# Kernel tuning notes

Hardware: AMD Instinct MI355X
Metric: run time of the kernel (lower is better)

## Reference

```python
import jax, jax.numpy as jnp
import numpy as np

V, T, E, HID = 32000, 48, 128, 256
B, L = 256, 512
H = HID // 2  # per-direction LSTM hidden


def setup_inputs() -> dict:
    key = jax.random.key(0)
    ks = jax.random.split(key, 16)
    lengths = jax.random.randint(ks[0], (B,), L // 2, L + 1)
    mask = (jnp.arange(L)[None, :] < lengths[:, None])  # (B, L) bool, step 0 always on
    words = jax.random.randint(ks[1], (B, L), 1, V).astype(jnp.int32)
    words = jnp.where(mask, words, 0)  # padding_idx = 0
    tags = jax.random.randint(ks[2], (B, L), 0, T).astype(jnp.int32)
    s = 0.1
    emb = jax.random.normal(ks[3], (V, E), jnp.float32) * s
    emb = emb.at[0].set(0.0)  # padding_idx row zeroed
    Wih_f = jax.random.normal(ks[4], (4 * H, E), jnp.float32) * s
    Whh_f = jax.random.normal(ks[5], (4 * H, H), jnp.float32) * s
    bih_f = jax.random.normal(ks[6], (4 * H,), jnp.float32) * s
    bhh_f = jax.random.normal(ks[7], (4 * H,), jnp.float32) * s
    Wih_b = jax.random.normal(ks[8], (4 * H, E), jnp.float32) * s
    Whh_b = jax.random.normal(ks[9], (4 * H, H), jnp.float32) * s
    bih_b = jax.random.normal(ks[10], (4 * H,), jnp.float32) * s
    bhh_b = jax.random.normal(ks[11], (4 * H,), jnp.float32) * s
    Wout = jax.random.normal(ks[12], (T, HID), jnp.float32) * s
    bout = jax.random.normal(ks[13], (T,), jnp.float32) * s
    trans = jax.random.normal(ks[14], (T, T), jnp.float32) * s
    se = jax.random.normal(ks[15], (2, T), jnp.float32) * s
    return dict(words=words, tags=tags, mask=mask, emb=emb,
                Wih_f=Wih_f, Whh_f=Whh_f, bih_f=bih_f, bhh_f=bhh_f,
                Wih_b=Wih_b, Whh_b=Whh_b, bih_b=bih_b, bhh_b=bhh_b,
                Wout=Wout, bout=bout, trans=trans,
                start_trans=se[0], end_trans=se[1])


def _lstm_dir(x, Wih, Whh, bih, bhh, reverse):
    # x: (L, B, E) -> hs: (L, B, H); PyTorch gate order i, f, g, o
    Lx, Bx, _ = x.shape
    Hx = Whh.shape[1]
    def step(carry, xt):
        h, c = carry
        g = xt @ Wih.T + h @ Whh.T + (bih + bhh)
        i, f, gg, o = jnp.split(g, 4, axis=-1)
        c = jax.nn.sigmoid(f) * c + jax.nn.sigmoid(i) * jnp.tanh(gg)
        h = jax.nn.sigmoid(o) * jnp.tanh(c)
        return (h, c), h
    init = (jnp.zeros((Bx, Hx), x.dtype), jnp.zeros((Bx, Hx), x.dtype))
    _, hs = jax.lax.scan(step, init, x, reverse=reverse)
    return hs


def reference(words, tags, mask, emb, Wih_f, Whh_f, bih_f, bhh_f,
              Wih_b, Whh_b, bih_b, bhh_b, Wout, bout, trans,
              start_trans, end_trans):
    Bn = words.shape[0]
    # --- features: embedding -> BiLSTM -> linear ---
    x = emb[words].transpose(1, 0, 2)          # (L, B, E)
    h_f = _lstm_dir(x, Wih_f, Whh_f, bih_f, bhh_f, reverse=False)
    h_b = _lstm_dir(x, Wih_b, Whh_b, bih_b, bhh_b, reverse=True)
    h = jnp.concatenate([h_f, h_b], axis=-1)   # (L, B, 2H)
    emis = h @ Wout.T + bout                   # (L, B, T)
    mT = mask.T                                # (L, B) bool
    mF = mT.astype(emis.dtype)
    tT = tags.T.astype(jnp.int32)              # (L, B)

    # --- CRF numerator: score of gold path ---
    barange = jnp.arange(Bn)
    num0 = start_trans[tT[0]] + emis[0, barange, tT[0]]
    def num_step(score, inp):
        em_t, tag_prev, tag_t, m_t = inp
        step_score = trans[tag_prev, tag_t] + em_t[barange, tag_t]
        return score + step_score * m_t, None
    num, _ = jax.lax.scan(num_step, num0, (emis[1:], tT[:-1], tT[1:], mF[1:]))
    seq_ends = mF.sum(0).astype(jnp.int32) - 1
    last_tags = tT[seq_ends, barange]
    num = num + end_trans[last_tags]

    # --- CRF denominator: forward algorithm (logsumexp recurrence) ---
    den0 = start_trans[None, :] + emis[0]      # (B, T)
    def den_step(score, inp):
        em_t, m_t = inp
        nxt = jax.nn.logsumexp(score[:, :, None] + trans[None] + em_t[:, None, :], axis=1)
        return jnp.where(m_t[:, None], nxt, score), None
    den, _ = jax.lax.scan(den_step, den0, (emis[1:], mT[1:]))
    denom = jax.nn.logsumexp(den + end_trans[None, :], axis=1)

    llh = num - denom
    return -llh.mean()  # reduction='mean', negated
```

## Files before the change

kernel.cpp:

```cpp
#include <hip/hip_runtime.h>
#include <hip/hip_bf16.h>

typedef unsigned short ushort_t;
typedef unsigned int uint_t;
typedef __bf16 bf16x8 __attribute__((ext_vector_type(8)));
typedef float f32x4 __attribute__((ext_vector_type(4)));

#define L2E 1.44269504088896340736f
#define LN2 0.69314718055994530942f

#define WGBAR() __asm__ volatile("s_waitcnt lgkmcnt(0)\n\ts_barrier" ::: "memory")

static __device__ __forceinline__ float fexp2(float x) { return __builtin_amdgcn_exp2f(x); }
static __device__ __forceinline__ float flog2(float x) { return __builtin_amdgcn_logf(x); }
static __device__ __forceinline__ float frcp (float x) { return __builtin_amdgcn_rcpf(x); }

static __device__ __forceinline__ float sigm(float x) {
  return frcp(1.0f + fexp2(-L2E * x));
}
static __device__ __forceinline__ float tanha(float x) {
  return 1.0f - 2.0f * frcp(1.0f + fexp2(2.0f * L2E * x));
}

static __device__ __forceinline__ uint_t cvtpk(float lo, float hi) {
  uint_t r;
  asm("v_cvt_pk_bf16_f32 %0, %1, %2" : "=v"(r) : "v"(lo), "v"(hi));
  return r;
}
static __device__ __forceinline__ bf16x8 pack8(float4 a, float4 b) {
  uint4 u = make_uint4(cvtpk(a.x, a.y), cvtpk(a.z, a.w),
                       cvtpk(b.x, b.y), cvtpk(b.z, b.w));
  return __builtin_bit_cast(bf16x8, u);
}
static __device__ __forceinline__ uint2 pack4(float4 a) {
  return make_uint2(cvtpk(a.x, a.y), cvtpk(a.z, a.w));
}

template <int K>
static __device__ __forceinline__ float rotk(float x) {
  if constexpr (K == 0) {
    return x;
  } else {
    return __builtin_bit_cast(float, __builtin_amdgcn_update_dpp(
        0, __builtin_bit_cast(int, x), 0x120 + K, 0xf, 0xf, true));
  }
}

__global__ __launch_bounds__(512, 2) void k2_lstm(
    const int* __restrict__ words, const float* __restrict__ emb,
    const float* __restrict__ Wih_f, const float* __restrict__ Whh_f,
    const float* __restrict__ bih_f, const float* __restrict__ bhh_f,
    const float* __restrict__ Wih_b, const float* __restrict__ Whh_b,
    const float* __restrict__ bih_b, const float* __restrict__ bhh_b,
    ushort_t* __restrict__ hT, float* __restrict__ loss_out) {
  const int wg = blockIdx.x;
  const int dir = wg >> 7;
  const int r0 = (wg & 127) << 1;
  if (wg == 0 && threadIdx.x == 0) loss_out[0] = 0.f;
  const float* Whh = dir ? Whh_b : Whh_f;
  const float* Wih = dir ? Wih_b : Wih_f;
  const float* bih = dir ? bih_b : bih_f;
  const float* bhh = dir ? bhh_b : bhh_f;

  const int tid = threadIdx.x;
  const int w = tid >> 6;
  const int lane = tid & 63;
  const int l15 = lane & 15;
  const int kq = lane >> 4;

  __shared__ __align__(16) ushort_t hx[2][2][136];
  __shared__ __align__(16) ushort_t xp[2][16][128][4];
  __shared__ __align__(16) ushort_t xs[2][16][136];

  bf16x8 wfh[4][4], wfx[4][4];
  float biasP[4];
#pragma unroll
  for (int Q = 0; Q < 4; ++Q) {
    const int n = Q * 128 + w * 16 + l15;
    biasP[Q] = bih[n] + bhh[n];
#pragma unroll
    for (int c = 0; c < 4; ++c) {
      const int k0 = c * 32 + kq * 8;
      const float* sh = Whh + n * 128 + k0;
      const float* sx = Wih + n * 128 + k0;
      wfh[Q][c] = pack8(*(const float4*)sh, *(const float4*)(sh + 4));
      wfx[Q][c] = pack8(*(const float4*)sx, *(const float4*)(sx + 4));
    }
  }

  const int ur = (lane >> 4) & 1;
  const int uj = w * 16 + l15;
  float cst = 0.f;
  const f32x4 fz = {0.f, 0.f, 0.f, 0.f};

  const int sm = tid >> 5;
  const int sc = (tid & 31) * 4;
  const int str = r0 + (sm & 1);
  const int stl = sm >> 1;

  uint_t pd0[4], pd1[4];
  f32x4 pc = {0.f, 0.f, 0.f, 0.f};
  f32x4 pcsv = {0.f, 0.f, 0.f, 0.f};

  if (tid < 256) hx[0][tid >> 7][tid & 127] = 0;
  {
    const int tg = stl;
    const int tf = dir ? (511 - tg) : tg;
    const int word = words[str * 512 + tf];
    float4 av = *(const float4*)(emb + (size_t)word * 128 + sc);
    *(uint2*)&xs[1][sm][sc] = pack4(av);
  }
  WGBAR();
  {
    f32x4 qv[4];
#pragma unroll
    for (int Q = 0; Q < 4; ++Q) {
      f32x4 pc0 = {biasP[Q], biasP[Q], biasP[Q], biasP[Q]};
#pragma unroll
      for (int c = 0; c < 4; ++c) {
        bf16x8 af = __builtin_bit_cast(bf16x8, *(const uint4*)&xs[1][l15][kq * 8 + c * 32]);
        pc0 = __builtin_amdgcn_mfma_f32_16x16x32_bf16(af, wfx[Q][c], pc0, 0, 0, 0);
      }
      qv[Q] = pc0;
    }
#pragma unroll
    for (int rr = 0; rr < 4; ++rr) {
      pd0[rr] = cvtpk(qv[0][rr], qv[1][rr]);
      pd1[rr] = cvtpk(qv[2][rr], qv[3][rr]);
      *(uint2*)&xp[0][kq * 4 + rr][uj][0] = make_uint2(pd0[rr], pd1[rr]);
    }
  }
  {
    const int tg = 8 + stl;
    const int tf = dir ? (511 - tg) : tg;
    const int word = words[str * 512 + tf];
    float4 av = *(const float4*)(emb + (size_t)word * 128 + sc);
    *(uint2*)&xs[0][sm][sc] = pack4(av);
  }
  WGBAR();

  int sword = 0;
  float4 se0 = make_float4(0.f, 0.f, 0.f, 0.f);

#pragma unroll 1
  for (int i = 0; i < 64; ++i) {
    const int pcon = i & 1;
    const int ppro = pcon ^ 1;
    bf16x8 afp[4];
    if (i < 63) {
#pragma unroll
      for (int c = 0; c < 4; ++c)
        afp[c] = __builtin_bit_cast(bf16x8, *(const uint4*)&xs[pcon][l15][kq * 8 + c * 32]);
    }
#pragma unroll
    for (int s = 0; s < 8; ++s) {
      const int t = i * 8 + s;
      const int p = t & 1;
      const uint2 xq = *(const uint2*)&xp[pcon][2 * s + ur][uj][0];
      if (i < 62) {
        if (s == 0) {
          const int tg = (i + 2) * 8 + stl;
          const int tf = dir ? (511 - tg) : tg;
          sword = words[str * 512 + tf];
        }
        if (s == 2) se0 = *(const float4*)(emb + (size_t)sword * 128 + sc);
        if (s == 6) *(uint2*)&xs[ppro][sm][sc] = pack4(se0);
      }
      f32x4 a0, a1, a2, a3;
      const ushort_t* abase = &hx[p][l15 & 1][kq * 8];
      {
        bf16x8 af = __builtin_bit_cast(bf16x8, *(const uint4*)(abase));
        a0 = __builtin_amdgcn_mfma_f32_16x16x32_bf16(af, wfh[0][0], fz, 0, 0, 0);
        a1 = __builtin_amdgcn_mfma_f32_16x16x32_bf16(af, wfh[1][0], fz, 0, 0, 0);
        a2 = __builtin_amdgcn_mfma_f32_16x16x32_bf16(af, wfh[2][0], fz, 0, 0, 0);
        a3 = __builtin_amdgcn_mfma_f32_16x16x32_bf16(af, wfh[3][0], fz, 0, 0, 0);
      }
#pragma unroll
      for (int c = 1; c < 4; ++c) {
        bf16x8 af = __builtin_bit_cast(bf16x8, *(const uint4*)(abase + c * 32));
        a0 = __builtin_amdgcn_mfma_f32_16x16x32_bf16(af, wfh[0][c], a0, 0, 0, 0);
        a1 = __builtin_amdgcn_mfma_f32_16x16x32_bf16(af, wfh[1][c], a1, 0, 0, 0);
        a2 = __builtin_amdgcn_mfma_f32_16x16x32_bf16(af, wfh[2][c], a2, 0, 0, 0);
        a3 = __builtin_amdgcn_mfma_f32_16x16x32_bf16(af, wfh[3][c], a3, 0, 0, 0);
      }
      if (i < 63) {
        const int Q = s >> 1;
        if ((s & 1) == 0) {
          pc = f32x4{biasP[Q], biasP[Q], biasP[Q], biasP[Q]};
          pc = __builtin_amdgcn_mfma_f32_16x16x32_bf16(afp[0], wfx[Q][0], pc, 0, 0, 0);
          pc = __builtin_amdgcn_mfma_f32_16x16x32_bf16(afp[1], wfx[Q][1], pc, 0, 0, 0);
        } else {
          pc = __builtin_amdgcn_mfma_f32_16x16x32_bf16(afp[2], wfx[Q][2], pc, 0, 0, 0);
          pc = __builtin_amdgcn_mfma_f32_16x16x32_bf16(afp[3], wfx[Q][3], pc, 0, 0, 0);
          if ((s & 2) == 0) {
            pcsv = pc;
          } else if (s == 3) {
#pragma unroll
            for (int rr = 0; rr < 4; ++rr) pd0[rr] = cvtpk(pcsv[rr], pc[rr]);
          } else {
#pragma unroll
            for (int rr = 0; rr < 4; ++rr) {
              pd1[rr] = cvtpk(pcsv[rr], pc[rr]);
              *(uint2*)&xp[ppro][kq * 4 + rr][uj][0] = make_uint2(pd0[rr], pd1[rr]);
            }
          }
        }
      }
      const float g0 = (ur ? a0[1] : a0[0]) + __builtin_bit_cast(float, xq.x << 16);
      const float g1 = (ur ? a1[1] : a1[0]) + __builtin_bit_cast(float, xq.x & 0xffff0000u);
      const float g2 = (ur ? a2[1] : a2[0]) + __builtin_bit_cast(float, xq.y << 16);
      const float g3 = (ur ? a3[1] : a3[0]) + __builtin_bit_cast(float, xq.y & 0xffff0000u);
      const float si = sigm(g0), sf = sigm(g1), so = sigm(g3);
      const float tg = tanha(g2);
      cst = sf * cst + si * tg;
      const float h = so * tanha(cst);
      const ushort_t hb = (ushort_t)cvtpk(h, h);
      if (lane < 32) {
        hx[p ^ 1][ur][uj] = hb;
        const int tf = dir ? (511 - t) : t;
        hT[((size_t)(r0 + ur) * 512 + tf) * 256 + (dir << 7) + uj] = hb;
      }
      WGBAR();
    }
  }
}

#define K4_ROW(OP, m) \
  OP(m, 0) OP(m, 1) OP(m, 2) OP(m, 3) OP(m, 4) OP(m, 5) OP(m, 6) OP(m, 7) \
  OP(m, 8) OP(m, 9) OP(m, 10) OP(m, 11) OP(m, 12) OP(m, 13) OP(m, 14) OP(m, 15)
#define K4_ALL(OP) K4_ROW(OP, 0) K4_ROW(OP, 1) K4_ROW(OP, 2) K4_ROW(OP, 3)

#define ROTMOD_0  ""
#define ROTMOD_1  "row_ror:1 row_mask:0xf bank_mask:0xf"
#define ROTMOD_2  "row_ror:2 row_mask:0xf bank_mask:0xf"
#define ROTMOD_3  "row_ror:3 row_mask:0xf bank_mask:0xf"
#define ROTMOD_4  "row_ror:4 row_mask:0xf bank_mask:0xf"
#define ROTMOD_5  "row_ror:5 row_mask:0xf bank_mask:0xf"
#define ROTMOD_6  "row_ror:6 row_mask:0xf bank_mask:0xf"
#define ROTMOD_7  "row_ror:7 row_mask:0xf bank_mask:0xf"
#define ROTMOD_8  "row_ror:8 row_mask:0xf bank_mask:0xf"
#define ROTMOD_9  "row_ror:9 row_mask:0xf bank_mask:0xf"
#define ROTMOD_10 "row_ror:10 row_mask:0xf bank_mask:0xf"
#define ROTMOD_11 "row_ror:11 row_mask:0xf bank_mask:0xf"
#define ROTMOD_12 "row_ror:12 row_mask:0xf bank_mask:0xf"
#define ROTMOD_13 "row_ror:13 row_mask:0xf bank_mask:0xf"
#define ROTMOD_14 "row_ror:14 row_mask:0xf bank_mask:0xf"
#define ROTMOD_15 "row_ror:15 row_mask:0xf bank_mask:0xf"

#define K4_FMA(m_, k_) asm( \
    "v_fmac_f32 %0, %1, %2 " ROTMOD_##k_ \
    : "+v"(acc[((m_) * 16 + (k_)) & 7]) \
    : "v"(dm[m_]), "v"(pcr[(m_) * 16 + (k_)]));

#define EMA(tt) tA[((tt) >> 6) & 1][(tt) & 63][jj]
#define EMB(tt) tB[((((tt) >> 6) & 1)) ^ 1][(tt) & 63][jj]

#define A_BODY(FOLD, TN, MEAS)                                                \
  {                                                                           \
    float E = Ecur;                                                           \
    if (FOLD) {                                                               \
      E *= __builtin_bit_cast(float, (uint_t)(127 - e_pend) << 23);           \
      S += e_pend;                                                            \
    }                                                                         \
    const float emn_ = EMA(TN);                                               \
    float dm[4];                                                              \
    dm[0] = d;                                                                \
    dm[1] = __shfl_xor(d, 16, 64);                                            \
    dm[2] = __shfl_xor(d, 32, 64);                                            \
    dm[3] = __shfl_xor(d, 48, 64);                                            \
    float acc[8] = {0.f, 0.f, 0.f, 0.f, 0.f, 0.f, 0.f, 0.f};                  \
    K4_ALL(K4_FMA)                                                            \
    d = (((acc[0] + acc[1]) + (acc[2] + acc[3])) +                            \
         ((acc[4] + acc[5]) + (acc[6] + acc[7]))) * E;                        \
    if (MEAS) {                                                               \
      const int db_ =                                                         \
          __builtin_amdgcn_readfirstlane(__builtin_bit_cast(int, d));         \
      e_pend = ((db_ >> 23) & 0xff) - 127;                                    \
    }                                                                         \
    Ecur = fexp2(emn_ * L2E);                                                 \
  }

#define B_BODY(FOLD, TN, MBIT, MEAS)                                          \
  {                                                                           \
    float E = Ecur;                                                           \
    int eApp = 0;                                                             \
    if (FOLD) {                                                               \
      E *= __builtin_bit_cast(float, (uint_t)(127 - e_pend) << 23);           \
      eApp = e_pend;                                                          \
    }                                                                         \
    const float emn_ = EMB(TN);                                               \
    const float vs = E * d;                                                   \
    float dm[4];                                                              \
    dm[0] = vs;                                                               \
    dm[1] = __shfl_xor(vs, 16, 64);                                           \
    dm[2] = __shfl_xor(vs, 32, 64);                                           \
    dm[3] = __shfl_xor(vs, 48, 64);                                           \
    float acc[8] = {0.f, 0.f, 0.f, 0.f, 0.f, 0.f, 0.f, 0.f};                  \
    K4_ALL(K4_FMA)                                                            \
    const float nxt = (((acc[0] + acc[1]) + (acc[2] + acc[3])) +              \
                       ((acc[4] + acc[5]) + (acc[6] + acc[7])));              \
    if (MBIT) { d = nxt; S += eApp; }                                         \
    if (MEAS) {                                                               \
      const int db_ =                                                         \
          __builtin_amdgcn_readfirstlane(__builtin_bit_cast(int, d));         \
      e_pend = ((db_ >> 23) & 0xff) - 127;                                    \
    }                                                                         \
    Ecur = fexp2(emn_ * L2E);                                                 \
  }

__global__ __launch_bounds__(128, 1) void k4_fused(
    const int* __restrict__ words, const int* __restrict__ tags,
    const ushort_t* __restrict__ hT, const float* __restrict__ Wout,
    const float* __restrict__ bout, const float* __restrict__ trans,
    const float* __restrict__ st, const float* __restrict__ et,
    float* __restrict__ out) {
  const int b = blockIdx.x;
  const int tid = threadIdx.x;
  const int wv = tid >> 6;
  const int lane = tid & 63;
  const int l15 = lane & 15;
  const int kq = lane >> 4;

  __shared__ __align__(16) ushort_t wfrag[3][8][64][8];
  __shared__ float tA[2][64][50];
  __shared__ float tB[2][64][50];
  __shared__ float shx[64];
  __shared__ float shmisc[2];

  const ushort_t* hb_base = hT + (size_t)b * 512 * 256;
  const int j = lane;
  const bool v = j < 48;
  const int jj = v ? j : 47;

  float bo3[3];
#pragma unroll
  for (int jt = 0; jt < 3; ++jt) bo3[jt] = bout[jt * 16 + l15];
#pragma unroll 1
  for (int f = wv; f < 24; f += 2) {
    const int jt = f >> 3, c = f & 7;
    const float* src = Wout + (jt * 16 + l15) * 256 + c * 32 + kq * 8;
    bf16x8 fr = pack8(*(const float4*)src, *(const float4*)(src + 4));
    *(uint4*)&wfrag[jt][c][lane][0] = __builtin_bit_cast(uint4, fr);
  }

  float pcr[64];
  {
    float pm[4];
    const float pj = (float)j;
    pm[0] = pj;
    pm[1] = __shfl_xor(pj, 16, 64);
    pm[2] = __shfl_xor(pj, 32, 64);
    pm[3] = __shfl_xor(pj, 48, 64);
    if (wv == 0) {
#define K4_CALF(m, k) { const int idx_ = (int)rotk<k>(pm[m]); \
      pcr[(m) * 16 + (k)] = (v && idx_ < 48) ? fexp2(trans[idx_ * 48 + j] * L2E) : 0.f; }
      K4_ALL(K4_CALF)
#undef K4_CALF
    } else {
#define K4_CALB(m, k) { const int idx_ = (int)rotk<k>(pm[m]); \
      pcr[(m) * 16 + (k)] = (v && idx_ < 48) ? fexp2(trans[j * 48 + idx_] * L2E) : 0.f; }
      K4_ALL(K4_CALB)
#undef K4_CALB
    }
  }

  unsigned long long mq4 = 0, mq5 = 0, mq6 = 0, mq7 = 0;
  if (wv == 1) {
    mq4 = __ballot(words[b * 512 + 4 * 64 + lane] != 0);
    mq5 = __ballot(words[b * 512 + 5 * 64 + lane] != 0);
    mq6 = __ballot(words[b * 512 + 6 * 64 + lane] != 0);
    mq7 = __ballot(words[b * 512 + 7 * 64 + lane] != 0);
  }
  __syncthreads();

  auto produce = [&](int tile, float (*dst)[50]) {
#pragma unroll
    for (int ts = 0; ts < 4; ++ts) {
      const int tt0 = tile * 64 + ts * 16;
      bf16x8 afr[8];
#pragma unroll
      for (int c = 0; c < 8; ++c)
        afr[c] = __builtin_bit_cast(bf16x8,
            *(const uint4*)(hb_base + (size_t)(tt0 + l15) * 256 + c * 32 + kq * 8));
#pragma unroll
      for (int jt = 0; jt < 3; ++jt) {
        f32x4 a2 = {bo3[jt], bo3[jt], bo3[jt], bo3[jt]};
#pragma unroll
        for (int c = 0; c < 8; ++c) {
          bf16x8 bfr = __builtin_bit_cast(bf16x8, *(const uint4*)&wfrag[jt][c][lane][0]);
          a2 = __builtin_amdgcn_mfma_f32_16x16x32_bf16(afr[c], bfr, a2, 0, 0, 0);
        }
#pragma unroll
        for (int r = 0; r < 4; ++r)
          dst[ts * 16 + kq * 4 + r][jt * 16 + l15] = a2[r];
      }
    }
  };

  if (wv == 0) produce(0, tA[0]); else produce(7, tB[0]);
  __syncthreads();

  float d, Ecur;
  int S = 0, e_pend = 0;
  float snum = 0.f;
  if (wv == 0) {
    d = v ? fexp2((st[j] + tA[0][0][jj]) * L2E) : 0.f;
    Ecur = fexp2(tA[0][1][jj] * L2E);
  } else {
    d = v ? fexp2(et[j] * L2E) : 0.f;
    Ecur = fexp2(tB[0][63][jj] * L2E);
  }

#pragma unroll 1
  for (int p = 0; p < 4; ++p) {
    if (wv == 0) {
      if (p < 3) produce(p + 1, tA[(p + 1) & 1]);
      {
        const int t = p * 64 + lane;
        const int tg = tags[b * 512 + t];
        if (t == 0) {
          snum += st[tg] + tA[0][0][tg];
        } else {
          const int tp = tags[b * 512 + t - 1];
          snum += trans[tp * 48 + tg] + tA[p & 1][lane][tg];
        }
      }
    } else {
      if (p < 3) produce(6 - p, tB[((6 - p) & 1) ^ 1]);
      {
        const int tl = 7 - p;
        const int t = tl * 64 + lane;
        const unsigned long long mqq =
            (p == 0) ? mq7 : (p == 1) ? mq6 : (p == 2) ? mq5 : mq4;
        if ((mqq >> lane) & 1ull) {
          const int tg = tags[b * 512 + t];
          const int tp = tags[b * 512 + t - 1];
          snum += trans[tp * 48 + tg] + tB[(tl & 1) ^ 1][lane][tg];
        }
      }
    }
    __syncthreads();
    if (wv == 0) {
      if (p == 0) {
        A_BODY(false, 2, false)
        A_BODY(true,  3, false)
        A_BODY(false, 4, false)
        A_BODY(false, 5, false)
        A_BODY(false, 6, false)
        A_BODY(false, 7, false)
        A_BODY(false, 8, false)
      }
#pragma unroll 1
      for (int gi = (p == 0) ? 1 : 0; gi < 8; ++gi) {
        const int G = p * 64 + gi * 8;
        A_BODY(false, G + 1, true)
        A_BODY(false, G + 2, false)
        A_BODY(true,  G + 3, false)
        A_BODY(false, G + 4, false)
        A_BODY(false, G + 5, false)
        A_BODY(false, G + 6, false)
        A_BODY(false, G + 7, false)
        A_BODY(false, min(G + 8, 255), false)
      }
    } else {
      const unsigned long long mq =
          (p == 0) ? mq7 : (p == 1) ? mq6 : (p == 2) ? mq5 : mq4;
#pragma unroll 1
      for (int gi = 0; gi < 8; ++gi) {
        const int t0 = 511 - p * 64 - gi * 8;
        const uint_t mm = (uint_t)(mq >> (56 - 8 * gi));
        B_BODY(false, t0 - 1, (mm >> 7) & 1u, true)
        B_BODY(false, t0 - 2, (mm >> 6) & 1u, false)
        B_BODY(true,  t0 - 3, (mm >> 5) & 1u, false)
        B_BODY(false, t0 - 4, (mm >> 4) & 1u, false)
        B_BODY(false, t0 - 5, (mm >> 3) & 1u, false)
        B_BODY(false, t0 - 6, (mm >> 2) & 1u, false)
        B_BODY(false, t0 - 7, (mm >> 1) & 1u, false)
        B_BODY(false, max(t0 - 8, 256), (mm >> 0) & 1u, false)
      }
    }
    __syncthreads();
  }

  if (wv == 0) {
    float sr = snum;
#pragma unroll
    for (int dd = 32; dd; dd >>= 1) sr += __shfl_xor(sr, dd, 64);
    shx[j] = d;
    if (lane == 0) { shmisc[0] = (float)S; shmisc[1] = sr; }
  }
  __syncthreads();
  if (wv == 1) {
    float uf = d * shx[j];
    float sr = snum;
#pragma unroll
    for (int dd = 32; dd; dd >>= 1) {
      uf += __shfl_xor(uf, dd, 64);
      sr += __shfl_xor(sr, dd, 64);
    }
    if (lane == 0) {
      const int cnt = 256 + (int)(__popcll(mq4) + __popcll(mq5) +
                                  __popcll(mq6) + __popcll(mq7));
      const int lt = tags[b * 512 + cnt - 1];
      const float num = shmisc[1] + sr + et[lt];
      const float denom = (shmisc[0] + (float)S + flog2(uf)) * LN2;
      atomicAdd(out, (denom - num) * (1.0f / 256.0f));
    }
  }
}

extern "C" void kernel_launch(void* const* d_in, const int* in_sizes, int n_in,
                              void* d_out, int out_size, void* d_ws, size_t ws_size,
                              hipStream_t stream) {
  (void)in_sizes; (void)n_in; (void)out_size; (void)ws_size;
  const int*   words = (const int*)d_in[0];
  const int*   tags  = (const int*)d_in[1];
  const float* emb   = (const float*)d_in[3];
  const float* Wih_f = (const float*)d_in[4];
  const float* Whh_f = (const float*)d_in[5];
  const float* bih_f = (const float*)d_in[6];
  const float* bhh_f = (const float*)d_in[7];
  const float* Wih_b = (const float*)d_in[8];
  const float* Whh_b = (const float*)d_in[9];
  const float* bih_b = (const float*)d_in[10];
  const float* bhh_b = (const float*)d_in[11];
  const float* Wout  = (const float*)d_in[12];
  const float* bout  = (const float*)d_in[13];
  const float* trans = (const float*)d_in[14];
  const float* st    = (const float*)d_in[15];
  const float* et    = (const float*)d_in[16];

  char* ws = (char*)d_ws;
  ushort_t* h_T = (ushort_t*)(ws);

  k2_lstm  <<<256, 512, 0, stream>>>(words, emb,
                                     Wih_f, Whh_f, bih_f, bhh_f,
                                     Wih_b, Whh_b, bih_b, bhh_b,
                                     h_T, (float*)d_out);
  k4_fused <<<256, 128, 0, stream>>>(words, tags, h_T, Wout, bout,
                                     trans, st, et, (float*)d_out);
}
```

Before: 447.5 us.

## Run forward and backward CRF recurrences interleaved in one wave, offload producer to other

The CRF kernel previously split the forward (alpha) and backward (beta) exp-space recurrences across two waves, with emission production interleaved and a barrier between phases. Now wave 0 runs both recurrences, interleaving A and B steps to hide each other's dependency latency. Wave 1 takes over emission tile production, the gold-path score and Wout fragment staging, and production now overlaps with the recurrence instead of sitting between barriers. The dot product is cut from 64 to 48 lanes and uses ds_bpermute instead of shfl_xor, which raises register pressure from holding two 48-entry transition tables in one wave.

```diff
diff --git a/kernel.cpp b/kernel.cpp
--- a/kernel.cpp
+++ b/kernel.cpp
@@ -44,6 +44,9 @@
     return __builtin_bit_cast(float, __builtin_amdgcn_update_dpp(
         0, __builtin_bit_cast(int, x), 0x120 + K, 0xf, 0xf, true));
   }
+}
+static __device__ __forceinline__ float bperf(int addr, int val) {
+  return __builtin_bit_cast(float, __builtin_amdgcn_ds_bpermute(addr, val));
 }
 
 __global__ __launch_bounds__(512, 2) void k2_lstm(
@@ -224,11 +227,6 @@
     }
   }
 }
-
-#define K4_ROW(OP, m) \
-  OP(m, 0) OP(m, 1) OP(m, 2) OP(m, 3) OP(m, 4) OP(m, 5) OP(m, 6) OP(m, 7) \
-  OP(m, 8) OP(m, 9) OP(m, 10) OP(m, 11) OP(m, 12) OP(m, 13) OP(m, 14) OP(m, 15)
-#define K4_ALL(OP) K4_ROW(OP, 0) K4_ROW(OP, 1) K4_ROW(OP, 2) K4_ROW(OP, 3)
 
 #define ROTMOD_0  ""
 #define ROTMOD_1  "row_ror:1 row_mask:0xf bank_mask:0xf"
@@ -247,66 +245,91 @@
 #define ROTMOD_14 "row_ror:14 row_mask:0xf bank_mask:0xf"
 #define ROTMOD_15 "row_ror:15 row_mask:0xf bank_mask:0xf"
 
-#define K4_FMA(m_, k_) asm( \
+#define K4_ROW16(OP, m) \
+  OP(m, 0) OP(m, 1) OP(m, 2) OP(m, 3) OP(m, 4) OP(m, 5) OP(m, 6) OP(m, 7) \
+  OP(m, 8) OP(m, 9) OP(m, 10) OP(m, 11) OP(m, 12) OP(m, 13) OP(m, 14) OP(m, 15)
+#define K4_S48(OP) K4_ROW16(OP, 0) K4_ROW16(OP, 1) K4_ROW16(OP, 2)
+
+#define K4_FMA_A(m_, k_) asm( \
     "v_fmac_f32 %0, %1, %2 " ROTMOD_##k_ \
     : "+v"(acc[((m_) * 16 + (k_)) & 7]) \
-    : "v"(dm[m_]), "v"(pcr[(m_) * 16 + (k_)]));
+    : "v"(dm##m_), "v"(pcr_a[(m_) * 16 + (k_)]));
+#define K4_FMA_B(m_, k_) asm( \
+    "v_fmac_f32 %0, %1, %2 " ROTMOD_##k_ \
+    : "+v"(acc[((m_) * 16 + (k_)) & 7]) \
+    : "v"(dm##m_), "v"(pcr_b[(m_) * 16 + (k_)]));
 
 #define EMA(tt) tA[((tt) >> 6) & 1][(tt) & 63][jj]
 #define EMB(tt) tB[((((tt) >> 6) & 1)) ^ 1][(tt) & 63][jj]
 
 #define A_BODY(FOLD, TN, MEAS)                                                \
   {                                                                           \
-    float E = Ecur;                                                           \
+    float E = Ecur_a;                                                         \
     if (FOLD) {                                                               \
-      E *= __builtin_bit_cast(float, (uint_t)(127 - e_pend) << 23);           \
-      S += e_pend;                                                            \
+      E *= __builtin_bit_cast(float, (uint_t)(127 - ep_a) << 23);             \
+      S_a += ep_a;                                                            \
     }                                                                         \
     const float emn_ = EMA(TN);                                               \
-    float dm[4];                                                              \
-    dm[0] = d;                                                                \
-    dm[1] = __shfl_xor(d, 16, 64);                                            \
-    dm[2] = __shfl_xor(d, 32, 64);                                            \
-    dm[3] = __shfl_xor(d, 48, 64);                                            \
+    const int di_ = __builtin_bit_cast(int, d_a);                             \
+    float dm0 = bperf(ba0, di_);                                              \
+    float dm1 = bperf(ba1, di_);                                              \
+    float dm2 = bperf(ba2, di_);                                              \
     float acc[8] = {0.f, 0.f, 0.f, 0.f, 0.f, 0.f, 0.f, 0.f};                  \
-    K4_ALL(K4_FMA)                                                            \
-    d = (((acc[0] + acc[1]) + (acc[2] + acc[3])) +                            \
-         ((acc[4] + acc[5]) + (acc[6] + acc[7]))) * E;                        \
+    K4_S48(K4_FMA_A)                                                          \
+    d_a = (((acc[0] + acc[1]) + (acc[2] + acc[3])) +                          \
+           ((acc[4] + acc[5]) + (acc[6] + acc[7]))) * E;                      \
     if (MEAS) {                                                               \
       const int db_ =                                                         \
-          __builtin_amdgcn_readfirstlane(__builtin_bit_cast(int, d));         \
-      e_pend = ((db_ >> 23) & 0xff) - 127;                                    \
+          __builtin_amdgcn_readfirstlane(__builtin_bit_cast(int, d_a));       \
+      ep_a = ((db_ >> 23) & 0xff) - 127;                                      \
     }                                                                         \
-    Ecur = fexp2(emn_ * L2E);                                                 \
+    Ecur_a = fexp2(emn_ * L2E);                                               \
   }
 
 #define B_BODY(FOLD, TN, MBIT, MEAS)                                          \
   {                                                                           \
-    float E = Ecur;                                                           \
+    float E = Ecur_b;                                                         \
     int eApp = 0;                                                             \
     if (FOLD) {                                                               \
-      E *= __builtin_bit_cast(float, (uint_t)(127 - e_pend) << 23);           \
-      eApp = e_pend;                                                          \
+      E *= __builtin_bit_cast(float, (uint_t)(127 - ep_b) << 23);             \
+      eApp = ep_b;                                                            \
     }                                                                         \
     const float emn_ = EMB(TN);                                               \
-    const float vs = E * d;                                                   \
-    float dm[4];                                                              \
-    dm[0] = vs;                                                               \
-    dm[1] = __shfl_xor(vs, 16, 64);                                           \
-    dm[2] = __shfl_xor(vs, 32, 64);                                           \
-    dm[3] = __shfl_xor(vs, 48, 64);                                           \
+    const float vs_ = E * d_b;                                                \
+    const int di_ = __builtin_bit_cast(int, vs_);                             \
+    float dm0 = bperf(ba0, di_);                                              \
+    float dm1 = bperf(ba1, di_);                                              \
+    float dm2 = bperf(ba2, di_);                                              \
     float acc[8] = {0.f, 0.f, 0.f, 0.f, 0.f, 0.f, 0.f, 0.f};                  \
-    K4_ALL(K4_FMA)                                                            \
-    const float nxt = (((acc[0] + acc[1]) + (acc[2] + acc[3])) +              \
-                       ((acc[4] + acc[5]) + (acc[6] + acc[7])));              \
-    if (MBIT) { d = nxt; S += eApp; }                                         \
+    K4_S48(K4_FMA_B)                                                          \
+    const float nxt_ = (((acc[0] + acc[1]) + (acc[2] + acc[3])) +             \
+                        ((acc[4] + acc[5]) + (acc[6] + acc[7])));             \
+    if (MBIT) { d_b = nxt_; S_b += eApp; }                                    \
     if (MEAS) {                                                               \
       const int db_ =                                                         \
-          __builtin_amdgcn_readfirstlane(__builtin_bit_cast(int, d));         \
-      e_pend = ((db_ >> 23) & 0xff) - 127;                                    \
+          __builtin_amdgcn_readfirstlane(__builtin_bit_cast(int, d_b));       \
+      ep_b = ((db_ >> 23) & 0xff) - 127;                                      \
     }                                                                         \
-    Ecur = fexp2(emn_ * L2E);                                                 \
-  }
+    Ecur_b = fexp2(emn_ * L2E);                                               \
+  }
+
+#define GROUP_PAIR(G, T0, MM)                                                 \
+  A_BODY(false, (G) + 1, true)                                                \
+  B_BODY(false, (T0) - 1, ((MM) >> 7) & 1u, true)                             \
+  A_BODY(false, (G) + 2, false)                                               \
+  B_BODY(false, (T0) - 2, ((MM) >> 6) & 1u, false)                            \
+  A_BODY(true,  (G) + 3, false)                                               \
+  B_BODY(true,  (T0) - 3, ((MM) >> 5) & 1u, false)                            \
+  A_BODY(false, (G) + 4, false)                                               \
+  B_BODY(false, (T0) - 4, ((MM) >> 4) & 1u, false)                            \
+  A_BODY(false, (G) + 5, false)                                               \
+  B_BODY(false, (T0) - 5, ((MM) >> 3) & 1u, false)                            \
+  A_BODY(false, (G) + 6, false)                                               \
+  B_BODY(false, (T0) - 6, ((MM) >> 2) & 1u, false)                            \
+  A_BODY(false, (G) + 7, false)                                               \
+  B_BODY(false, (T0) - 7, ((MM) >> 1) & 1u, false)                            \
+  A_BODY(false, ALAST, false)                                                 \
+  B_BODY(false, BLAST, ((MM) >> 0) & 1u, false)
 
 __global__ __launch_bounds__(128, 1) void k4_fused(
     const int* __restrict__ words, const int* __restrict__ tags,
@@ -324,52 +347,48 @@
   __shared__ __align__(16) ushort_t wfrag[3][8][64][8];
   __shared__ float tA[2][64][50];
   __shared__ float tB[2][64][50];
-  __shared__ float shx[64];
-  __shared__ float shmisc[2];
+  __shared__ float res1[1];
 
   const ushort_t* hb_base = hT + (size_t)b * 512 * 256;
   const int j = lane;
   const bool v = j < 48;
   const int jj = v ? j : 47;
 
+  const int ba0 = 4 * (0 * 16 + l15);
+  const int ba1 = 4 * (1 * 16 + l15);
+  const int ba2 = 4 * (2 * 16 + l15);
+
   float bo3[3];
 #pragma unroll
   for (int jt = 0; jt < 3; ++jt) bo3[jt] = bout[jt * 16 + l15];
-#pragma unroll 1
-  for (int f = wv; f < 24; f += 2) {
-    const int jt = f >> 3, c = f & 7;
-    const float* src = Wout + (jt * 16 + l15) * 256 + c * 32 + kq * 8;
-    bf16x8 fr = pack8(*(const float4*)src, *(const float4*)(src + 4));
-    *(uint4*)&wfrag[jt][c][lane][0] = __builtin_bit_cast(uint4, fr);
-  }
-
-  float pcr[64];
-  {
-    float pm[4];
-    const float pj = (float)j;
-    pm[0] = pj;
-    pm[1] = __shfl_xor(pj, 16, 64);
-    pm[2] = __shfl_xor(pj, 32, 64);
-    pm[3] = __shfl_xor(pj, 48, 64);
-    if (wv == 0) {
-#define K4_CALF(m, k) { const int idx_ = (int)rotk<k>(pm[m]); \
-      pcr[(m) * 16 + (k)] = (v && idx_ < 48) ? fexp2(trans[idx_ * 48 + j] * L2E) : 0.f; }
-      K4_ALL(K4_CALF)
-#undef K4_CALF
-    } else {
-#define K4_CALB(m, k) { const int idx_ = (int)rotk<k>(pm[m]); \
-      pcr[(m) * 16 + (k)] = (v && idx_ < 48) ? fexp2(trans[j * 48 + idx_] * L2E) : 0.f; }
-      K4_ALL(K4_CALB)
+
+  float pcr_a[48], pcr_b[48];
+  unsigned long long mq4 = 0, mq5 = 0, mq6 = 0, mq7 = 0;
+  if (wv == 0) {
+    const int pj = __builtin_bit_cast(int, (float)j);
+    float pm0 = bperf(ba0, pj);
+    float pm1 = bperf(ba1, pj);
+    float pm2 = bperf(ba2, pj);
+#define K4_CALA(m, k) { const int idx_ = (int)rotk<k>(pm##m); \
+    pcr_a[(m) * 16 + (k)] = (v && idx_ < 48) ? fexp2(trans[idx_ * 48 + j] * L2E) : 0.f; }
+    K4_S48(K4_CALA)
+#undef K4_CALA
+#define K4_CALB(m, k) { const int idx_ = (int)rotk<k>(pm##m); \
+    pcr_b[(m) * 16 + (k)] = (v && idx_ < 48) ? fexp2(trans[j * 48 + idx_] * L2E) : 0.f; }
+    K4_S48(K4_CALB)
 #undef K4_CALB
-    }
-  }
-
-  unsigned long long mq4 = 0, mq5 = 0, mq6 = 0, mq7 = 0;
-  if (wv == 1) {
     mq4 = __ballot(words[b * 512 + 4 * 64 + lane] != 0);
     mq5 = __ballot(words[b * 512 + 5 * 64 + lane] != 0);
     mq6 = __ballot(words[b * 512 + 6 * 64 + lane] != 0);
     mq7 = __ballot(words[b * 512 + 7 * 64 + lane] != 0);
+  } else {
+#pragma unroll 1
+    for (int f = 0; f < 24; ++f) {
+      const int jt = f / 8, c = f & 7;
+      const float* src = Wout + (jt * 16 + l15) * 256 + c * 32 + kq * 8;
+      bf16x8 fr = pack8(*(const float4*)src, *(const float4*)(src + 4));
+      *(uint4*)&wfrag[jt][c][lane][0] = __builtin_bit_cast(uint4, fr);
+    }
   }
   __syncthreads();
 
@@ -397,24 +416,68 @@
     }
   };
 
-  if (wv == 0) produce(0, tA[0]); else produce(7, tB[0]);
+  unsigned long long nb4 = 0, nb5 = 0, nb6 = 0, nb7 = 0;
+  float snum = 0.f;
+  if (wv == 1) {
+    nb4 = __ballot(words[b * 512 + 4 * 64 + lane] != 0);
+    nb5 = __ballot(words[b * 512 + 5 * 64 + lane] != 0);
+    nb6 = __ballot(words[b * 512 + 6 * 64 + lane] != 0);
+    nb7 = __ballot(words[b * 512 + 7 * 64 + lane] != 0);
+    produce(0, tA[0]);
+    produce(7, tB[0]);
+  }
   __syncthreads();
 
-  float d, Ecur;
-  int S = 0, e_pend = 0;
-  float snum = 0.f;
+  float d_a = 0.f, Ecur_a = 0.f, d_b = 0.f, Ecur_b = 0.f;
+  int S_a = 0, ep_a = 0, S_b = 0, ep_b = 0;
   if (wv == 0) {
-    d = v ? fexp2((st[j] + tA[0][0][jj]) * L2E) : 0.f;
-    Ecur = fexp2(tA[0][1][jj] * L2E);
-  } else {
-    d = v ? fexp2(et[j] * L2E) : 0.f;
-    Ecur = fexp2(tB[0][63][jj] * L2E);
+    d_a = v ? fexp2((st[j] + tA[0][0][jj]) * L2E) : 0.f;
+    Ecur_a = fexp2(tA[0][1][jj] * L2E);
+    d_b = v ? fexp2(et[j] * L2E) : 0.f;
+    Ecur_b = fexp2(tB[0][63][jj] * L2E);
   }
 
 #pragma unroll 1
   for (int p = 0; p < 4; ++p) {
     if (wv == 0) {
-      if (p < 3) produce(p + 1, tA[(p + 1) & 1]);
+      const unsigned long long mq =
+          (p == 0) ? mq7 : (p == 1) ? mq6 : (p == 2) ? mq5 : mq4;
+      if (p > 0) {
+        Ecur_a = fexp2(EMA(64 * p) * L2E);
+        Ecur_b = fexp2(EMB(511 - 64 * p) * L2E);
+      }
+      if (p == 0) {
+        const uint_t mm = (uint_t)(mq >> 56);
+        A_BODY(false, 2, false)
+        B_BODY(false, 510, (mm >> 7) & 1u, true)
+        A_BODY(true,  3, false)
+        B_BODY(false, 509, (mm >> 6) & 1u, false)
+        A_BODY(false, 4, false)
+        B_BODY(true,  508, (mm >> 5) & 1u, false)
+        A_BODY(false, 5, false)
+        B_BODY(false, 507, (mm >> 4) & 1u, false)
+        A_BODY(false, 6, false)
+        B_BODY(false, 506, (mm >> 3) & 1u, false)
+        A_BODY(false, 7, false)
+        B_BODY(false, 505, (mm >> 2) & 1u, false)
+        A_BODY(false, 8, false)
+        B_BODY(false, 504, (mm >> 1) & 1u, false)
+        B_BODY(false, 503, (mm >> 0) & 1u, false)
+      }
+#pragma unroll 1
+      for (int gi = (p == 0) ? 1 : 0; gi < 8; ++gi) {
+        const int G = p * 64 + gi * 8;
+        const int T0 = 511 - p * 64 - gi * 8;
+        const uint_t mm = (uint_t)(mq >> (56 - 8 * gi));
+        const int ALAST = (gi == 7) ? (p * 64 + 63) : (G + 8);
+        const int BLAST = (gi == 7) ? (448 - p * 64) : (T0 - 8);
+        GROUP_PAIR(G, T0, mm)
+      }
+    } else {
+      if (p < 3) {
+        produce(p + 1, tA[(p + 1) & 1]);
+        produce(6 - p, tB[((6 - p) & 1) ^ 1]);
+      }
       {
         const int t = p * 64 + lane;
         const int tg = tags[b * 512 + t];
@@ -425,13 +488,11 @@
           snum += trans[tp * 48 + tg] + tA[p & 1][lane][tg];
         }
       }
-    } else {
-      if (p < 3) produce(6 - p, tB[((6 - p) & 1) ^ 1]);
       {
         const int tl = 7 - p;
         const int t = tl * 64 + lane;
         const unsigned long long mqq =
-            (p == 0) ? mq7 : (p == 1) ? mq6 : (p == 2) ? mq5 : mq4;
+            (p == 0) ? nb7 : (p == 1) ? nb6 : (p == 2) ? nb5 : nb4;
         if ((mqq >> lane) & 1ull) {
           const int tg = tags[b * 512 + t];
           const int tp = tags[b * 512 + t - 1];
@@ -440,71 +501,27 @@
       }
     }
     __syncthreads();
-    if (wv == 0) {
-      if (p == 0) {
-        A_BODY(false, 2, false)
-        A_BODY(true,  3, false)
-        A_BODY(false, 4, false)
-        A_BODY(false, 5, false)
-        A_BODY(false, 6, false)
-        A_BODY(false, 7, false)
-        A_BODY(false, 8, false)
-      }
-#pragma unroll 1
-      for (int gi = (p == 0) ? 1 : 0; gi < 8; ++gi) {
-        const int G = p * 64 + gi * 8;
-        A_BODY(false, G + 1, true)
-        A_BODY(false, G + 2, false)
-        A_BODY(true,  G + 3, false)
-        A_BODY(false, G + 4, false)
-        A_BODY(false, G + 5, false)
-        A_BODY(false, G + 6, false)
-        A_BODY(false, G + 7, false)
-        A_BODY(false, min(G + 8, 255), false)
-      }
-    } else {
-      const unsigned long long mq =
-          (p == 0) ? mq7 : (p == 1) ? mq6 : (p == 2) ? mq5 : mq4;
-#pragma unroll 1
-      for (int gi = 0; gi < 8; ++gi) {
-        const int t0 = 511 - p * 64 - gi * 8;
-        const uint_t mm = (uint_t)(mq >> (56 - 8 * gi));
-        B_BODY(false, t0 - 1, (mm >> 7) & 1u, true)
-        B_BODY(false, t0 - 2, (mm >> 6) & 1u, false)
-        B_BODY(true,  t0 - 3, (mm >> 5) & 1u, false)
-        B_BODY(false, t0 - 4, (mm >> 4) & 1u, false)
-        B_BODY(false, t0 - 5, (mm >> 3) & 1u, false)
-        B_BODY(false, t0 - 6, (mm >> 2) & 1u, false)
-        B_BODY(false, t0 - 7, (mm >> 1) & 1u, false)
-        B_BODY(false, max(t0 - 8, 256), (mm >> 0) & 1u, false)
-      }
-    }
-    __syncthreads();
-  }
-
+  }
+
+  if (wv == 1) {
+    float sr = snum;
+#pragma unroll
+    for (int dd = 32; dd; dd >>= 1) sr += __shfl_xor(sr, dd, 64);
+    if (lane == 0) {
+      const int cnt = 256 + (int)(__popcll(nb4) + __popcll(nb5) +
+                                  __popcll(nb6) + __popcll(nb7));
+      const int lt = tags[b * 512 + cnt - 1];
+      res1[0] = sr + et[lt];
+    }
+  }
+  __syncthreads();
   if (wv == 0) {
-    float sr = snum;
-#pragma unroll
-    for (int dd = 32; dd; dd >>= 1) sr += __shfl_xor(sr, dd, 64);
-    shx[j] = d;
-    if (lane == 0) { shmisc[0] = (float)S; shmisc[1] = sr; }
-  }
-  __syncthreads();
-  if (wv == 1) {
-    float uf = d * shx[j];
-    float sr = snum;
-#pragma unroll
-    for (int dd = 32; dd; dd >>= 1) {
-      uf += __shfl_xor(uf, dd, 64);
-      sr += __shfl_xor(sr, dd, 64);
-    }
+    float uf = d_a * d_b;
+#pragma unroll
+    for (int dd = 32; dd; dd >>= 1) uf += __shfl_xor(uf, dd, 64);
     if (lane == 0) {
-      const int cnt = 256 + (int)(__popcll(mq4) + __popcll(mq5) +
-                                  __popcll(mq6) + __popcll(mq7));
-      const int lt = tags[b * 512 + cnt - 1];
-      const float num = shmisc[1] + sr + et[lt];
-      const float denom = (shmisc[0] + (float)S + flog2(uf)) * LN2;
-      atomicAdd(out, (denom - num) * (1.0f / 256.0f));
+      const float denom = ((float)(S_a + S_b) + flog2(uf)) * LN2;
+      atomicAdd(out, (denom - res1[0]) * (1.0f / 256.0f));
     }
   }
 }
```

Measured after the change: 477.1 us. 6.6% more time.
